# Performance work log

Hardware: AMD Instinct MI355X
Metric: run time of the kernel (lower is better)

Reference implementation:

```python
import jax, jax.numpy as jnp
import numpy as np

ALPHA = 0.2  # LeakyReLU negative slope
MASK_VAL = -1e9


def setup_inputs() -> dict:
    key = jax.random.key(0)
    k1, k2, k3, k4 = jax.random.split(key, 4)
    B, N, F_in, F_out = 8, 2048, 512, 512
    h = jax.random.normal(k1, (B, N, F_in), dtype=jnp.float32)
    adj = jax.random.randint(k2, (B, N, N), 0, 2, dtype=jnp.int32)
    # xavier_uniform with gain=1.414
    def xavier(k, shape, gain=1.414):
        fan_in, fan_out = shape[0], shape[1]
        bound = gain * np.sqrt(6.0 / (fan_in + fan_out))
        return jax.random.uniform(k, shape, jnp.float32, -bound, bound)
    W = xavier(k3, (F_in, F_out))
    a = xavier(k4, (2 * F_out, 1))
    return {"h": h, "adj": adj, "W": W, "a": a}


def reference(h, adj, W, a):
    # h: [B,N,Fin], adj: [B,N,N], W: [Fin,Fout], a: [2*Fout,1]
    Fout = W.shape[1]
    Wh = jnp.matmul(h, W)  # [B,N,Fout]
    # Split 'a' into source/target halves: concat([Wh_i, Wh_j]) @ a
    #   == (Wh_i @ a1) + (Wh_j @ a2), avoiding the O(N^2*2F) concat tensor.
    a1 = a[:Fout, 0]   # [Fout]
    a2 = a[Fout:, 0]   # [Fout]
    e_i = jnp.einsum('bnf,f->bn', Wh, a1)  # [B,N] score contribution of node i
    e_j = jnp.einsum('bnf,f->bn', Wh, a2)  # [B,N] score contribution of node j
    e = e_i[:, :, None] + e_j[:, None, :]  # [B,N,N]
    e = jax.nn.leaky_relu(e, negative_slope=ALPHA)
    e = jnp.where(adj == 0, MASK_VAL, e)
    attention = jax.nn.softmax(e, axis=2)  # [B,N,N]
    h_prime = jnp.matmul(attention, Wh)    # [B,N,Fout]
    return jax.nn.elu(h_prime)
```

## Files before the change

kernel.cpp:

```cpp
#include <hip/hip_runtime.h>
#include <hip/hip_bf16.h>

#define ALPHA 0.2f
#define LOG2E 1.44269504088896340736f

typedef float  f32x4 __attribute__((ext_vector_type(4)));
typedef float  f32x2 __attribute__((ext_vector_type(2)));
typedef int    i32x4 __attribute__((ext_vector_type(4)));
typedef int    i32x2 __attribute__((ext_vector_type(2)));

static __device__ __forceinline__ void mfma_bf16_16x16x32(f32x4& c, i32x4 a, i32x4 b) {
  asm("v_mfma_f32_16x16x32_bf16 %0, %1, %2, %0" : "+v"(c) : "v"(a), "v"(b));
}

static __device__ __forceinline__ unsigned short f2bf(float x) {
  __hip_bfloat16 b = __float2bfloat16(x);
  return *reinterpret_cast<unsigned short*>(&b);
}
static __device__ __forceinline__ unsigned int packbf2(float x, float y) {
  return (unsigned int)f2bf(x) | ((unsigned int)f2bf(y) << 16);
}
static __device__ __forceinline__ float dot4(f32x4 a, f32x4 b) {
  return a.x*b.x + a.y*b.y + a.z*b.z + a.w*b.w;
}

__global__ __launch_bounds__(256) void k_setup(const float* __restrict__ W, const float* __restrict__ a,
                                               unsigned short* __restrict__ wt,
                                               float* __restrict__ v1, float* __restrict__ v2) {
  const int bid = blockIdx.x, tid = threadIdx.x;
  __shared__ float S[32][33];
  if (bid < 256) {
    const int k0 = (bid >> 4) * 32, f0 = (bid & 15) * 32;
    const int r = tid >> 5, c = tid & 31;
    #pragma unroll
    for (int rr = r; rr < 32; rr += 8) S[rr][c] = W[(size_t)(k0 + rr) * 512 + f0 + c];
    __syncthreads();
    #pragma unroll
    for (int rr = r; rr < 32; rr += 8) wt[(size_t)(f0 + rr) * 512 + k0 + c] = f2bf(S[c][rr]);
  } else {
    const int kk = (bid - 256) * 4 + (tid >> 6);
    const int l = tid & 63;
    const float* wr = W + (size_t)kk * 512 + l * 8;
    f32x4 w0 = *(const f32x4*)(wr),           w1 = *(const f32x4*)(wr + 4);
    f32x4 p0 = *(const f32x4*)(a + l*8),      p1 = *(const f32x4*)(a + l*8 + 4);
    f32x4 q0 = *(const f32x4*)(a + 512 + l*8),q1 = *(const f32x4*)(a + 512 + l*8 + 4);
    float s1 = dot4(w0,p0) + dot4(w1,p1);
    float s2 = dot4(w0,q0) + dot4(w1,q1);
    #pragma unroll
    for (int off = 1; off < 64; off <<= 1) { s1 += __shfl_xor(s1, off); s2 += __shfl_xor(s2, off); }
    if (l == 0) { v1[kk] = s1; v2[kk] = s2; }
  }
}

__global__ __launch_bounds__(256) void k_ei_ej(const float* __restrict__ h,
                                               const float* __restrict__ v1, const float* __restrict__ v2,
                                               float* __restrict__ ei, float* __restrict__ ej) {
  const int row = blockIdx.x * 4 + (threadIdx.x >> 6);
  const int l = threadIdx.x & 63;
  const float* hr = h + (size_t)row * 512 + l * 8;
  f32x4 x0 = *(const f32x4*)hr,            x1 = *(const f32x4*)(hr + 4);
  f32x4 a0 = *(const f32x4*)(v1 + l*8),    a1 = *(const f32x4*)(v1 + l*8 + 4);
  f32x4 b0 = *(const f32x4*)(v2 + l*8),    b1 = *(const f32x4*)(v2 + l*8 + 4);
  float s1 = dot4(x0,a0) + dot4(x1,a1);
  float s2 = dot4(x0,b0) + dot4(x1,b1);
  #pragma unroll
  for (int off = 1; off < 64; off <<= 1) { s1 += __shfl_xor(s1, off); s2 += __shfl_xor(s2, off); }
  if (l == 0) { ei[row] = s1 * LOG2E; ej[row] = s2 * LOG2E; }
}

__global__ __launch_bounds__(512, 2) void k_gemm_wh(const float* __restrict__ h,
                                                    const unsigned short* __restrict__ wt,
                                                    unsigned short* __restrict__ whT) {
  const int tid = threadIdx.x;
  const int w = tid >> 6, l = tid & 63;
  const int i0g = blockIdx.x * 64;
  const int b = i0g >> 11;
  const int nb = i0g & 2047;
  __shared__ __align__(16) unsigned short Alds[2][4][64][8];

  const int sr = tid >> 3;
  const int sc = (tid & 7) * 4;
  const float* hrow = h + (size_t)(i0g + sr) * 512 + sc;

  const int fl = l & 15, kq = l >> 4;
  const unsigned short* wp[4];
  #pragma unroll
  for (int cf = 0; cf < 4; ++cf) {
    const int f = w*64 + cf*16 + fl;
    wp[cf] = wt + (size_t)f * 512 + kq * 8;
  }

  f32x4 acc[4][4];
  #pragma unroll
  for (int i = 0; i < 4; ++i)
    #pragma unroll
    for (int j = 0; j < 4; ++j) acc[i][j] = (f32x4){0.f,0.f,0.f,0.f};

  f32x4 hcur = *(const f32x4*)hrow;
  i32x4 bcur[4];
  #pragma unroll
  for (int cf = 0; cf < 4; ++cf) bcur[cf] = *(const i32x4*)(wp[cf]);

  for (int s = 0; s < 16; ++s) {
    const unsigned int lo = packbf2(hcur.x, hcur.y), hi = packbf2(hcur.z, hcur.w);
    *(i32x2*)&Alds[s & 1][sc >> 3][sr][sc & 7] = (i32x2){(int)lo, (int)hi};
    const int sn = (s < 15) ? s + 1 : 15;
    if (s < 15) hcur = *(const f32x4*)(hrow + sn * 32);
    __syncthreads();
    i32x4 bnxt[4];
    #pragma unroll
    for (int cf = 0; cf < 4; ++cf) bnxt[cf] = *(const i32x4*)(wp[cf] + sn * 32);
    i32x4 af[4];
    #pragma unroll
    for (int fr = 0; fr < 4; ++fr) af[fr] = *(const i32x4*)&Alds[s & 1][kq][fr*16 + fl][0];
    #pragma unroll
    for (int fr = 0; fr < 4; ++fr)
      #pragma unroll
      for (int cf = 0; cf < 4; ++cf)
        mfma_bf16_16x16x32(acc[fr][cf], af[fr], bcur[cf]);
    #pragma unroll
    for (int cf = 0; cf < 4; ++cf) bcur[cf] = bnxt[cf];
  }

  asm volatile("s_nop 7\ns_nop 7\ns_nop 7" :::);
  const int il0 = kq * 4;
  #pragma unroll
  for (int fr = 0; fr < 4; ++fr) {
    #pragma unroll
    for (int cf = 0; cf < 4; ++cf) {
      const f32x4 v = acc[fr][cf];
      const int f = w*64 + cf*16 + fl;
      const int n = nb + fr*16 + il0;
      unsigned long long pk = (unsigned long long)packbf2(v.x, v.y)
                            | ((unsigned long long)packbf2(v.z, v.w) << 32);
      *(unsigned long long*)(whT + (size_t)(b*512 + f) * 2048 + n) = pk;
    }
  }
}

__global__ __launch_bounds__(512, 2) void k_attn(const int* __restrict__ adj,
                                                 const unsigned short* __restrict__ whT,
                                                 const float* __restrict__ ei, const float* __restrict__ ej,
                                                 float* __restrict__ out) {
  const int tid = threadIdx.x;
  const int w = tid >> 6, l = tid & 63;
  const int bid = blockIdx.x;
  const int b = bid >> 5;
  const int i0 = (bid & 31) * 64;

  __shared__ __align__(16) unsigned short Plds[2][64][40];
  __shared__ __align__(16) float ejl[2048];
  __shared__ __align__(16) float eil[64];
  __shared__ __align__(16) float llds[64];

  for (int idx = tid; idx < 2048; idx += 512) ejl[idx] = ej[b*2048 + idx];
  if (tid < 64) eil[tid] = ei[b*2048 + i0 + tid];
  __syncthreads();

  const int r = tid >> 4, c2 = tid & 15;
  const float eir0 = eil[r], eir1 = eil[r + 32];
  const int* adj0 = adj + (size_t)(b*2048 + i0 + r) * 2048 + c2*2;
  const int* adj1 = adj0 + (size_t)32 * 2048;

  const int fl = l & 15, kq = l >> 4;
  const unsigned short* wp[4];
  #pragma unroll
  for (int cf = 0; cf < 4; ++cf) {
    const int f = w*64 + cf*16 + fl;
    wp[cf] = whT + (size_t)(b*512 + f) * 2048 + kq*8;
  }

  f32x4 acc[4][4];
  #pragma unroll
  for (int i = 0; i < 4; ++i)
    #pragma unroll
    for (int j = 0; j < 4; ++j) acc[i][j] = (f32x4){0.f,0.f,0.f,0.f};
  float sum0 = 0.f, sum1 = 0.f;

  i32x2 a0c = *(const i32x2*)(adj0);
  i32x2 a1c = *(const i32x2*)(adj1);
  i32x4 bcur[4];
  #pragma unroll
  for (int cf = 0; cf < 4; ++cf) bcur[cf] = *(const i32x4*)(wp[cf]);

  for (int t = 0; t < 64; ++t) {
    const int tn = (t < 63) ? t + 1 : 63;
    i32x2 a0n = *(const i32x2*)(adj0 + tn*32);
    i32x2 a1n = *(const i32x2*)(adj1 + tn*32);
    i32x4 bnxt[4];
    #pragma unroll
    for (int cf = 0; cf < 4; ++cf) bnxt[cf] = *(const i32x4*)(wp[cf] + tn*32);

    const f32x2 ejv = *(const f32x2*)&ejl[t*32 + c2*2];
    float e00 = eir0 + ejv.x, e01 = eir0 + ejv.y;
    float e10 = eir1 + ejv.x, e11 = eir1 + ejv.y;
    e00 = fmaxf(e00, ALPHA*e00); e01 = fmaxf(e01, ALPHA*e01);
    e10 = fmaxf(e10, ALPHA*e10); e11 = fmaxf(e11, ALPHA*e11);
    const float p00 = a0c.x ? __builtin_amdgcn_exp2f(e00) : 0.f;
    const float p01 = a0c.y ? __builtin_amdgcn_exp2f(e01) : 0.f;
    const float p10 = a1c.x ? __builtin_amdgcn_exp2f(e10) : 0.f;
    const float p11 = a1c.y ? __builtin_amdgcn_exp2f(e11) : 0.f;
    sum0 += p00 + p01; sum1 += p10 + p11;
    *(unsigned int*)&Plds[t & 1][r][c2*2]      = packbf2(p00, p01);
    *(unsigned int*)&Plds[t & 1][r + 32][c2*2] = packbf2(p10, p11);
    __syncthreads();

    i32x4 af[4];
    #pragma unroll
    for (int fr = 0; fr < 4; ++fr) af[fr] = *(const i32x4*)&Plds[t & 1][fr*16 + fl][kq*8];
    #pragma unroll
    for (int fr = 0; fr < 4; ++fr)
      #pragma unroll
      for (int cf = 0; cf < 4; ++cf)
        mfma_bf16_16x16x32(acc[fr][cf], af[fr], bcur[cf]);

    #pragma unroll
    for (int cf = 0; cf < 4; ++cf) bcur[cf] = bnxt[cf];
    a0c = a0n; a1c = a1n;
  }

  #pragma unroll
  for (int off = 1; off < 16; off <<= 1) { sum0 += __shfl_xor(sum0, off); sum1 += __shfl_xor(sum1, off); }
  if (c2 == 0) { llds[r] = sum0; llds[r + 32] = sum1; }
  __syncthreads();
  asm volatile("s_nop 7\ns_nop 7\ns_nop 7" :::);

  #pragma unroll
  for (int fr = 0; fr < 4; ++fr) {
    const f32x4 lv = *(const f32x4*)&llds[fr*16 + kq*4];
    f32x4 inv;
    inv.x = __builtin_amdgcn_rcpf(lv.x); inv.y = __builtin_amdgcn_rcpf(lv.y);
    inv.z = __builtin_amdgcn_rcpf(lv.z); inv.w = __builtin_amdgcn_rcpf(lv.w);
    #pragma unroll
    for (int cf = 0; cf < 4; ++cf) {
      const int f = w*64 + cf*16 + fl;
      float* op = out + (size_t)(b*2048 + i0 + fr*16 + kq*4) * 512 + f;
      const f32x4 v = acc[fr][cf];
      float o0 = v.x * inv.x; o0 = o0 > 0.f ? o0 : __expf(o0) - 1.f; op[0]    = o0;
      float o1 = v.y * inv.y; o1 = o1 > 0.f ? o1 : __expf(o1) - 1.f; op[512]  = o1;
      float o2 = v.z * inv.z; o2 = o2 > 0.f ? o2 : __expf(o2) - 1.f; op[1024] = o2;
      float o3 = v.w * inv.w; o3 = o3 > 0.f ? o3 : __expf(o3) - 1.f; op[1536] = o3;
    }
  }
}

extern "C" void kernel_launch(void* const* d_in, const int* in_sizes, int n_in,
                              void* d_out, int out_size, void* d_ws, size_t ws_size,
                              hipStream_t stream) {
  const float* h  = (const float*)d_in[0];
  const int*  adj = (const int*)d_in[1];
  const float* W  = (const float*)d_in[2];
  const float* a  = (const float*)d_in[3];
  float* out = (float*)d_out;
  char* ws = (char*)d_ws;
  unsigned short* wt  = (unsigned short*)(ws);
  unsigned short* whT = (unsigned short*)(ws + 524288);
  float* ei = (float*)(ws + 524288 + 16777216);
  float* ej = ei + 16384;
  float* v1 = ej + 16384;
  float* v2 = v1 + 512;

  hipLaunchKernelGGL(k_setup,  dim3(384),  dim3(256), 0, stream, W, a, wt, v1, v2);
  hipLaunchKernelGGL(k_ei_ej,  dim3(4096), dim3(256), 0, stream, h, v1, v2, ei, ej);
  hipLaunchKernelGGL(k_gemm_wh,dim3(256),  dim3(512), 0, stream, h, wt, whT);
  hipLaunchKernelGGL(k_attn,   dim3(256),  dim3(512), 0, stream, adj, whT, ei, ej, out);
}
```

Baseline: 318.7 us.

## Fuse ei/ej into Wh GEMM, retile attention to 1024 threads, deeper prefetch

```diff
diff --git a/kernel.cpp b/kernel.cpp
--- a/kernel.cpp
+++ b/kernel.cpp
@@ -48,84 +48,79 @@
     float s2 = dot4(w0,q0) + dot4(w1,q1);
     #pragma unroll
     for (int off = 1; off < 64; off <<= 1) { s1 += __shfl_xor(s1, off); s2 += __shfl_xor(s2, off); }
-    if (l == 0) { v1[kk] = s1; v2[kk] = s2; }
-  }
-}
-
-__global__ __launch_bounds__(256) void k_ei_ej(const float* __restrict__ h,
-                                               const float* __restrict__ v1, const float* __restrict__ v2,
-                                               float* __restrict__ ei, float* __restrict__ ej) {
-  const int row = blockIdx.x * 4 + (threadIdx.x >> 6);
-  const int l = threadIdx.x & 63;
-  const float* hr = h + (size_t)row * 512 + l * 8;
-  f32x4 x0 = *(const f32x4*)hr,            x1 = *(const f32x4*)(hr + 4);
-  f32x4 a0 = *(const f32x4*)(v1 + l*8),    a1 = *(const f32x4*)(v1 + l*8 + 4);
-  f32x4 b0 = *(const f32x4*)(v2 + l*8),    b1 = *(const f32x4*)(v2 + l*8 + 4);
-  float s1 = dot4(x0,a0) + dot4(x1,a1);
-  float s2 = dot4(x0,b0) + dot4(x1,b1);
-  #pragma unroll
-  for (int off = 1; off < 64; off <<= 1) { s1 += __shfl_xor(s1, off); s2 += __shfl_xor(s2, off); }
-  if (l == 0) { ei[row] = s1 * LOG2E; ej[row] = s2 * LOG2E; }
-}
-
-__global__ __launch_bounds__(512, 2) void k_gemm_wh(const float* __restrict__ h,
+    if (l == 0) { v1[kk] = s1 * LOG2E; v2[kk] = s2 * LOG2E; }
+  }
+}
+
+__global__ __launch_bounds__(512, 4) void k_gemm_wh(const float* __restrict__ h,
                                                     const unsigned short* __restrict__ wt,
-                                                    unsigned short* __restrict__ whT) {
+                                                    const float* __restrict__ v1g, const float* __restrict__ v2g,
+                                                    unsigned short* __restrict__ whT,
+                                                    float* __restrict__ ei, float* __restrict__ ej) {
   const int tid = threadIdx.x;
   const int w = tid >> 6, l = tid & 63;
-  const int i0g = blockIdx.x * 64;
-  const int b = i0g >> 11;
-  const int nb = i0g & 2047;
-  __shared__ __align__(16) unsigned short Alds[2][4][64][8];
-
-  const int sr = tid >> 3;
-  const int sc = (tid & 7) * 4;
-  const float* hrow = h + (size_t)(i0g + sr) * 512 + sc;
+  const int n0g = blockIdx.x * 32;
+  const int b = n0g >> 11;
+  const int nb = n0g & 2047;
+  __shared__ __align__(16) unsigned short Al[2][32][36];
+  __shared__ float v1l[512], v2l[512];
+  v1l[tid] = v1g[tid]; v2l[tid] = v2g[tid];
+
+  const int sr = tid >> 4;
+  const int sc = (tid & 15) * 2;
+  const float* hrow = h + (size_t)(n0g + sr) * 512 + sc;
 
   const int fl = l & 15, kq = l >> 4;
   const unsigned short* wp[4];
   #pragma unroll
-  for (int cf = 0; cf < 4; ++cf) {
-    const int f = w*64 + cf*16 + fl;
-    wp[cf] = wt + (size_t)f * 512 + kq * 8;
-  }
-
-  f32x4 acc[4][4];
-  #pragma unroll
-  for (int i = 0; i < 4; ++i)
+  for (int cf = 0; cf < 4; ++cf) wp[cf] = wt + (size_t)(w*64 + cf*16 + fl) * 512 + kq * 8;
+
+  f32x4 acc[2][4];
+  #pragma unroll
+  for (int i = 0; i < 2; ++i)
     #pragma unroll
     for (int j = 0; j < 4; ++j) acc[i][j] = (f32x4){0.f,0.f,0.f,0.f};
-
-  f32x4 hcur = *(const f32x4*)hrow;
+  float s1 = 0.f, s2 = 0.f;
+
+  f32x2 hcur = __builtin_nontemporal_load((const f32x2*)hrow);
   i32x4 bcur[4];
   #pragma unroll
   for (int cf = 0; cf < 4; ++cf) bcur[cf] = *(const i32x4*)(wp[cf]);
-
+  __syncthreads();
+
+  #pragma unroll 2
   for (int s = 0; s < 16; ++s) {
-    const unsigned int lo = packbf2(hcur.x, hcur.y), hi = packbf2(hcur.z, hcur.w);
-    *(i32x2*)&Alds[s & 1][sc >> 3][sr][sc & 7] = (i32x2){(int)lo, (int)hi};
+    *(unsigned int*)&Al[s & 1][sr][sc] = packbf2(hcur.x, hcur.y);
     const int sn = (s < 15) ? s + 1 : 15;
-    if (s < 15) hcur = *(const f32x4*)(hrow + sn * 32);
+    f32x2 hnxt = __builtin_nontemporal_load((const f32x2*)(hrow + sn * 32));
+    i32x4 bnxt[4];
+    #pragma unroll
+    for (int cf = 0; cf < 4; ++cf) bnxt[cf] = *(const i32x4*)(wp[cf] + sn * 32);
+    const int k = s*32 + sc;
+    s1 += hcur.x * v1l[k] + hcur.y * v1l[k+1];
+    s2 += hcur.x * v2l[k] + hcur.y * v2l[k+1];
     __syncthreads();
-    i32x4 bnxt[4];
-    #pragma unroll
-    for (int cf = 0; cf < 4; ++cf) bnxt[cf] = *(const i32x4*)(wp[cf] + sn * 32);
-    i32x4 af[4];
-    #pragma unroll
-    for (int fr = 0; fr < 4; ++fr) af[fr] = *(const i32x4*)&Alds[s & 1][kq][fr*16 + fl][0];
-    #pragma unroll
-    for (int fr = 0; fr < 4; ++fr)
+    i32x4 af[2];
+    #pragma unroll
+    for (int fr = 0; fr < 2; ++fr) af[fr] = *(const i32x4*)&Al[s & 1][fr*16 + fl][kq*8];
+    #pragma unroll
+    for (int fr = 0; fr < 2; ++fr)
       #pragma unroll
       for (int cf = 0; cf < 4; ++cf)
         mfma_bf16_16x16x32(acc[fr][cf], af[fr], bcur[cf]);
     #pragma unroll
     for (int cf = 0; cf < 4; ++cf) bcur[cf] = bnxt[cf];
-  }
+    hcur = hnxt;
+  }
+
+  #pragma unroll
+  for (int off = 1; off < 16; off <<= 1) { s1 += __shfl_xor(s1, off); s2 += __shfl_xor(s2, off); }
+  if ((tid & 15) == 0) { ei[n0g + sr] = s1; ej[n0g + sr] = s2; }
 
   asm volatile("s_nop 7\ns_nop 7\ns_nop 7" :::);
   const int il0 = kq * 4;
   #pragma unroll
-  for (int fr = 0; fr < 4; ++fr) {
+  for (int fr = 0; fr < 2; ++fr) {
     #pragma unroll
     for (int cf = 0; cf < 4; ++cf) {
       const f32x4 v = acc[fr][cf];
@@ -138,71 +133,63 @@
   }
 }
 
-__global__ __launch_bounds__(512, 2) void k_attn(const int* __restrict__ adj,
-                                                 const unsigned short* __restrict__ whT,
-                                                 const float* __restrict__ ei, const float* __restrict__ ej,
-                                                 float* __restrict__ out) {
+__global__ __launch_bounds__(1024, 4) void k_attn(const int* __restrict__ adj,
+                                                  const unsigned short* __restrict__ whT,
+                                                  const float* __restrict__ ei, const float* __restrict__ ej,
+                                                  float* __restrict__ out) {
   const int tid = threadIdx.x;
   const int w = tid >> 6, l = tid & 63;
-  const int bid = blockIdx.x;
-  const int b = bid >> 5;
-  const int i0 = (bid & 31) * 64;
+  const int b = blockIdx.x & 7;
+  const int i0 = (blockIdx.x >> 3) * 64;
 
   __shared__ __align__(16) unsigned short Plds[2][64][40];
   __shared__ __align__(16) float ejl[2048];
   __shared__ __align__(16) float eil[64];
   __shared__ __align__(16) float llds[64];
 
-  for (int idx = tid; idx < 2048; idx += 512) ejl[idx] = ej[b*2048 + idx];
+  for (int idx = tid; idx < 2048; idx += 1024) ejl[idx] = ej[b*2048 + idx];
   if (tid < 64) eil[tid] = ei[b*2048 + i0 + tid];
   __syncthreads();
 
   const int r = tid >> 4, c2 = tid & 15;
-  const float eir0 = eil[r], eir1 = eil[r + 32];
+  const float eir = eil[r];
   const int* adj0 = adj + (size_t)(b*2048 + i0 + r) * 2048 + c2*2;
-  const int* adj1 = adj0 + (size_t)32 * 2048;
 
   const int fl = l & 15, kq = l >> 4;
-  const unsigned short* wp[4];
-  #pragma unroll
-  for (int cf = 0; cf < 4; ++cf) {
-    const int f = w*64 + cf*16 + fl;
-    wp[cf] = whT + (size_t)(b*512 + f) * 2048 + kq*8;
-  }
-
-  f32x4 acc[4][4];
+  const unsigned short* wp[2];
+  #pragma unroll
+  for (int cf = 0; cf < 2; ++cf) wp[cf] = whT + (size_t)(b*512 + w*32 + cf*16 + fl) * 2048 + kq*8;
+
+  f32x4 acc[4][2];
   #pragma unroll
   for (int i = 0; i < 4; ++i)
     #pragma unroll
-    for (int j = 0; j < 4; ++j) acc[i][j] = (f32x4){0.f,0.f,0.f,0.f};
-  float sum0 = 0.f, sum1 = 0.f;
-
-  i32x2 a0c = *(const i32x2*)(adj0);
-  i32x2 a1c = *(const i32x2*)(adj1);
-  i32x4 bcur[4];
-  #pragma unroll
-  for (int cf = 0; cf < 4; ++cf) bcur[cf] = *(const i32x4*)(wp[cf]);
-
+    for (int j = 0; j < 2; ++j) acc[i][j] = (f32x4){0.f,0.f,0.f,0.f};
+  float sum = 0.f;
+
+  i32x2 a0 = __builtin_nontemporal_load((const i32x2*)(adj0));
+  i32x2 a1 = __builtin_nontemporal_load((const i32x2*)(adj0 + 32));
+  i32x2 a2 = __builtin_nontemporal_load((const i32x2*)(adj0 + 64));
+  i32x4 b0[2], b1[2];
+  #pragma unroll
+  for (int cf = 0; cf < 2; ++cf) { b0[cf] = *(const i32x4*)(wp[cf]); b1[cf] = *(const i32x4*)(wp[cf] + 32); }
+
+  #pragma unroll 2
   for (int t = 0; t < 64; ++t) {
-    const int tn = (t < 63) ? t + 1 : 63;
-    i32x2 a0n = *(const i32x2*)(adj0 + tn*32);
-    i32x2 a1n = *(const i32x2*)(adj1 + tn*32);
-    i32x4 bnxt[4];
-    #pragma unroll
-    for (int cf = 0; cf < 4; ++cf) bnxt[cf] = *(const i32x4*)(wp[cf] + tn*32);
+    const int t2 = (t + 2 < 64) ? t + 2 : 63;
+    const int t3 = (t + 3 < 64) ? t + 3 : 63;
+    i32x2 an = __builtin_nontemporal_load((const i32x2*)(adj0 + t3*32));
+    i32x4 bn[2];
+    #pragma unroll
+    for (int cf = 0; cf < 2; ++cf) bn[cf] = *(const i32x4*)(wp[cf] + t2*32);
 
     const f32x2 ejv = *(const f32x2*)&ejl[t*32 + c2*2];
-    float e00 = eir0 + ejv.x, e01 = eir0 + ejv.y;
-    float e10 = eir1 + ejv.x, e11 = eir1 + ejv.y;
-    e00 = fmaxf(e00, ALPHA*e00); e01 = fmaxf(e01, ALPHA*e01);
-    e10 = fmaxf(e10, ALPHA*e10); e11 = fmaxf(e11, ALPHA*e11);
-    const float p00 = a0c.x ? __builtin_amdgcn_exp2f(e00) : 0.f;
-    const float p01 = a0c.y ? __builtin_amdgcn_exp2f(e01) : 0.f;
-    const float p10 = a1c.x ? __builtin_amdgcn_exp2f(e10) : 0.f;
-    const float p11 = a1c.y ? __builtin_amdgcn_exp2f(e11) : 0.f;
-    sum0 += p00 + p01; sum1 += p10 + p11;
-    *(unsigned int*)&Plds[t & 1][r][c2*2]      = packbf2(p00, p01);
-    *(unsigned int*)&Plds[t & 1][r + 32][c2*2] = packbf2(p10, p11);
+    float e0 = eir + ejv.x, e1 = eir + ejv.y;
+    e0 = fmaxf(e0, ALPHA*e0); e1 = fmaxf(e1, ALPHA*e1);
+    const float p0 = a0.x ? __builtin_amdgcn_exp2f(e0) : 0.f;
+    const float p1 = a0.y ? __builtin_amdgcn_exp2f(e1) : 0.f;
+    sum += p0 + p1;
+    *(unsigned int*)&Plds[t & 1][r][c2*2] = packbf2(p0, p1);
     __syncthreads();
 
     i32x4 af[4];
@@ -211,17 +198,17 @@
     #pragma unroll
     for (int fr = 0; fr < 4; ++fr)
       #pragma unroll
-      for (int cf = 0; cf < 4; ++cf)
-        mfma_bf16_16x16x32(acc[fr][cf], af[fr], bcur[cf]);
-
-    #pragma unroll
-    for (int cf = 0; cf < 4; ++cf) bcur[cf] = bnxt[cf];
-    a0c = a0n; a1c = a1n;
-  }
-
-  #pragma unroll
-  for (int off = 1; off < 16; off <<= 1) { sum0 += __shfl_xor(sum0, off); sum1 += __shfl_xor(sum1, off); }
-  if (c2 == 0) { llds[r] = sum0; llds[r + 32] = sum1; }
+      for (int cf = 0; cf < 2; ++cf)
+        mfma_bf16_16x16x32(acc[fr][cf], af[fr], b0[cf]);
+
+    #pragma unroll
+    for (int cf = 0; cf < 2; ++cf) { b0[cf] = b1[cf]; b1[cf] = bn[cf]; }
+    a0 = a1; a1 = a2; a2 = an;
+  }
+
+  #pragma unroll
+  for (int off = 1; off < 16; off <<= 1) sum += __shfl_xor(sum, off);
+  if (c2 == 0) llds[r] = sum;
   __syncthreads();
   asm volatile("s_nop 7\ns_nop 7\ns_nop 7" :::);
 
@@ -232,14 +219,18 @@
     inv.x = __builtin_amdgcn_rcpf(lv.x); inv.y = __builtin_amdgcn_rcpf(lv.y);
     inv.z = __builtin_amdgcn_rcpf(lv.z); inv.w = __builtin_amdgcn_rcpf(lv.w);
     #pragma unroll
-    for (int cf = 0; cf < 4; ++cf) {
-      const int f = w*64 + cf*16 + fl;
+    for (int cf = 0; cf < 2; ++cf) {
+      const int f = w*32 + cf*16 + fl;
       float* op = out + (size_t)(b*2048 + i0 + fr*16 + kq*4) * 512 + f;
       const f32x4 v = acc[fr][cf];
-      float o0 = v.x * inv.x; o0 = o0 > 0.f ? o0 : __expf(o0) - 1.f; op[0]    = o0;
-      float o1 = v.y * inv.y; o1 = o1 > 0.f ? o1 : __expf(o1) - 1.f; op[512]  = o1;
-      float o2 = v.z * inv.z; o2 = o2 > 0.f ? o2 : __expf(o2) - 1.f; op[1024] = o2;
-      float o3 = v.w * inv.w; o3 = o3 > 0.f ? o3 : __expf(o3) - 1.f; op[1536] = o3;
+      float o0 = v.x * inv.x; o0 = o0 > 0.f ? o0 : __expf(o0) - 1.f;
+      float o1 = v.y * inv.y; o1 = o1 > 0.f ? o1 : __expf(o1) - 1.f;
+      float o2 = v.z * inv.z; o2 = o2 > 0.f ? o2 : __expf(o2) - 1.f;
+      float o3 = v.w * inv.w; o3 = o3 > 0.f ? o3 : __expf(o3) - 1.f;
+      __builtin_nontemporal_store(o0, op);
+      __builtin_nontemporal_store(o1, op + 512);
+      __builtin_nontemporal_store(o2, op + 1024);
+      __builtin_nontemporal_store(o3, op + 1536);
     }
   }
 }
@@ -260,8 +251,7 @@
   float* v1 = ej + 16384;
   float* v2 = v1 + 512;
 
-  hipLaunchKernelGGL(k_setup,  dim3(384),  dim3(256), 0, stream, W, a, wt, v1, v2);
-  hipLaunchKernelGGL(k_ei_ej,  dim3(4096), dim3(256), 0, stream, h, v1, v2, ei, ej);
-  hipLaunchKernelGGL(k_gemm_wh,dim3(256),  dim3(512), 0, stream, h, wt, whT);
-  hipLaunchKernelGGL(k_attn,   dim3(256),  dim3(512), 0, stream, adj, whT, ei, ej, out);
-}
+  hipLaunchKernelGGL(k_setup,   dim3(384), dim3(256),  0, stream, W, a, wt, v1, v2);
+  hipLaunchKernelGGL(k_gemm_wh, dim3(512), dim3(512),  0, stream, h, wt, v1, v2, whT, ei, ej);
+  hipLaunchKernelGGL(k_attn,    dim3(256), dim3(1024), 0, stream, adj, whT, ei, ej, out);
+}
```

Measured after the change: 318.4 us. About the same (-0.1%).
